# Optimization experiments

Hardware: AMD Instinct MI355X
Metric: run time of the kernel (lower is better)

Reference implementation:

```python
import jax, jax.numpy as jnp
import numpy as np

B, N, M, NS = 4, 32768, 1024, 32
RADIUS = 0.1
EPS = 1e-5
CHANS = [16, 32, 32, 64]


def setup_inputs() -> dict:
    key = jax.random.key(0)
    ks = jax.random.split(key, 8)
    d = {
        'theta': jax.random.uniform(ks[0], (B, N), jnp.float32, 0.0, float(np.pi)),
        'phi': jax.random.uniform(ks[1], (B, N), jnp.float32, 0.0, 2.0 * float(np.pi)),
        'features': jax.random.normal(ks[2], (B, CHANS[0], N), jnp.float32),
    }
    for i, (ci, co) in enumerate(zip(CHANS[:-1], CHANS[1:])):
        d[f'w{i}'] = jax.random.normal(jax.random.fold_in(ks[3], i), (co, ci), jnp.float32) * 0.1
        d[f'b{i}'] = jnp.zeros((co,), jnp.float32)
        d[f'g{i}'] = jnp.ones((co,), jnp.float32)
        d[f'be{i}'] = jnp.zeros((co,), jnp.float32)
    return d


def _group(theta, phi, features):
    # angular ball query + random neighbor sampling (deterministic key),
    # duplicates padded with the first valid neighbor (max-pool invariant,
    # matching the torch code's sampling-with-replacement semantics).
    k1, k2 = jax.random.split(jax.random.key(42))
    n = theta.shape[1]
    cent_idx = jax.random.permutation(k1, n)[:M]                 # shared across batch, like torch code
    ct = theta[:, cent_idx]                                      # (B, M)
    cp = phi[:, cent_idx]
    th_s, ph_s = jax.lax.stop_gradient(theta), jax.lax.stop_gradient(phi)
    ct_s, cp_s = jax.lax.stop_gradient(ct), jax.lax.stop_gradient(cp)
    dist = jnp.sqrt((th_s[:, None, :] - ct_s[:, :, None]) ** 2 +
                    (ph_s[:, None, :] - cp_s[:, :, None]) ** 2)  # (B, M, N)
    mask = dist <= RADIUS
    scores = jnp.where(mask, jax.random.uniform(k2, dist.shape, jnp.float32), jnp.inf)
    _, idx = jax.lax.top_k(-scores, NS)                          # NS random in-ball indices, (B, M, NS)
    valid = jnp.take_along_axis(mask, idx, axis=-1)
    idx = jnp.where(valid, idx, idx[..., :1])                    # centroid itself is always valid at slot 0
    gathered = jax.vmap(lambda f, i: f[:, i])(features, idx)     # (B, C, M, NS)
    grouped = jnp.transpose(gathered, (0, 1, 3, 2))              # (B, C, NS, M)
    return ct, cp, grouped


def _mlp_max(x, params):
    # 1x1 conv + BatchNorm (batch stats, training mode) + ReLU stack, then max over nsample
    for w, b, g, be in params:
        x = jnp.einsum('oc,bcsm->bosm', w, x) + b[None, :, None, None]
        mu = x.mean(axis=(0, 2, 3), keepdims=True)
        var = x.var(axis=(0, 2, 3), keepdims=True)
        x = (x - mu) * jax.lax.rsqrt(var + EPS) * g[None, :, None, None] + be[None, :, None, None]
        x = jax.nn.relu(x)
    return x.max(axis=2)                                         # (B, C_out, M)


def reference(theta, phi, features, w0, b0, g0, be0, w1, b1, g1, be1, w2, b2, g2, be2):
    params = [(w0, b0, g0, be0), (w1, b1, g1, be1), (w2, b2, g2, be2)]
    ct, cp, grouped = _group(theta, phi, features)
    new_feats = _mlp_max(grouped, params)
    return ct, cp, new_feats
```

## Files before the change

kernel.cpp:

```cpp
#include <hip/hip_runtime.h>
#include <stdint.h>

#define N_PTS 32768
#define M_CENT 1024
#define B_SZ 4
#define NS 32
#define NR 64
#define P_TOT (B_SZ * NS * M_CENT)

#define GT 29
#define GP 58
#define NCELL (GT * GP)
#define INVF (1.0f / 0.11f)
#define CAPW 320

__device__ __forceinline__ int cell_t(float t) {
  return min(GT - 1, (int)(t * INVF));
}
__device__ __forceinline__ int cell_p(float p) {
  return min(GP - 1, (int)(p * INVF));
}

struct Key2 { uint32_t a, b; };

__device__ __forceinline__ uint32_t rotl32(uint32_t v, uint32_t r) {
  return (v << r) | (v >> (32u - r));
}

__device__ __forceinline__ void tf2x32(uint32_t k0, uint32_t k1,
                                       uint32_t& x0, uint32_t& x1) {
  uint32_t ks0 = k0, ks1 = k1, ks2 = k0 ^ k1 ^ 0x1BD11BDAu;
  x0 += ks0; x1 += ks1;
#define TF_ROUND(r) { x0 += x1; x1 = rotl32(x1, r); x1 ^= x0; }
  TF_ROUND(13u) TF_ROUND(15u) TF_ROUND(26u) TF_ROUND(6u)
  x0 += ks1; x1 += ks2 + 1u;
  TF_ROUND(17u) TF_ROUND(29u) TF_ROUND(16u) TF_ROUND(24u)
  x0 += ks2; x1 += ks0 + 2u;
  TF_ROUND(13u) TF_ROUND(15u) TF_ROUND(26u) TF_ROUND(6u)
  x0 += ks0; x1 += ks1 + 3u;
  TF_ROUND(17u) TF_ROUND(29u) TF_ROUND(16u) TF_ROUND(24u)
  x0 += ks1; x1 += ks2 + 4u;
  TF_ROUND(13u) TF_ROUND(15u) TF_ROUND(26u) TF_ROUND(6u)
  x0 += ks2; x1 += ks0 + 5u;
#undef TF_ROUND
}

__device__ __forceinline__ Key2 tf_block(Key2 k, uint32_t hi, uint32_t lo) {
  uint32_t x0 = hi, x1 = lo;
  tf2x32(k.a, k.b, x0, x1);
  Key2 r; r.a = x0; r.b = x1; return r;
}

__global__ __launch_bounds__(256) void prep_kernel(const float* __restrict__ theta,
                                                   const float* __restrict__ phi,
                                                   uint32_t* __restrict__ bits1,
                                                   uint32_t* __restrict__ bits2,
                                                   int* __restrict__ hist1,
                                                   int* __restrict__ hist2,
                                                   int* __restrict__ cellcnt) {
  int j = blockIdx.x * 256 + threadIdx.x;
  int b = j >> 15;
  float t = theta[j], p = phi[j];
  atomicAdd(&cellcnt[b * NCELL + cell_t(t) * GP + cell_p(p)], 1);
  if (j < N_PTS) {
    Key2 root; root.a = 0u; root.b = 42u;
    Key2 k1   = tf_block(root, 0u, 0u);
    Key2 keyA = tf_block(k1, 0u, 0u);
    Key2 sub1 = tf_block(k1, 0u, 1u);
    Key2 sub2 = tf_block(keyA, 0u, 1u);
    Key2 r1 = tf_block(sub1, 0u, (uint32_t)j);
    Key2 r2 = tf_block(sub2, 0u, (uint32_t)j);
    uint32_t v1 = r1.a ^ r1.b, v2 = r2.a ^ r2.b;
    bits1[j] = v1; bits2[j] = v2;
    atomicAdd(&hist1[v1 >> 16], 1);
    atomicAdd(&hist2[v2 >> 16], 1);
  }
}

__global__ __launch_bounds__(256) void transpose_kernel(const float* __restrict__ feat,
                                                        float* __restrict__ featT) {
  __shared__ float lds[16][65];
  int b = blockIdx.y;
  int n0 = blockIdx.x * 64;
  int tid = threadIdx.x;
#pragma unroll
  for (int k = 0; k < 4; ++k) {
    int v = tid + k * 256;
    int c = v >> 6, no = v & 63;
    lds[c][no] = feat[((size_t)(b * 16 + c) << 15) + n0 + no];
  }
  __syncthreads();
#pragma unroll
  for (int k = 0; k < 4; ++k) {
    int v = tid + k * 256;
    int no = v >> 4, c = v & 15;
    featT[((size_t)(b << 15) + n0 + no) * 16 + c] = lds[c][no];
  }
}

__global__ __launch_bounds__(256) void scans_kernel(const int* __restrict__ hist1,
                                                    const int* __restrict__ hist2,
                                                    int* __restrict__ gbase1,
                                                    int* __restrict__ gbase2,
                                                    const int* __restrict__ cellcnt,
                                                    int* __restrict__ cellpre,
                                                    int* __restrict__ cellcur) {
  __shared__ int s[256];
  int t = threadIdx.x;
  if (blockIdx.x < 2) {
    const int* hist = blockIdx.x == 0 ? hist1 : hist2;
    int* gbase = blockIdx.x == 0 ? gbase1 : gbase2;
    int sum = 0;
    for (int i = 0; i < 256; ++i) sum += hist[t * 256 + i];
    s[t] = sum;
    __syncthreads();
    if (t == 0) {
      int run = 0;
      for (int i = 0; i < 256; ++i) { int v = s[i]; s[i] = run; run += v; }
    }
    __syncthreads();
    gbase[t] = s[t];
  } else {
    int b = blockIdx.x - 2;
    const int* cnt = cellcnt + b * NCELL;
    int i0 = t * 7, i1 = min(i0 + 7, NCELL);
    int sum = 0;
    for (int i = i0; i < i1; ++i) sum += cnt[i];
    s[t] = sum;
    __syncthreads();
    for (int off = 1; off < 256; off <<= 1) {
      int v = (t >= off) ? s[t - off] : 0;
      __syncthreads();
      s[t] += v;
      __syncthreads();
    }
    int run = (t == 0) ? 0 : s[t - 1];
    for (int i = i0; i < i1; ++i) {
      cellpre[b * NCELL + i] = run;
      cellcur[b * NCELL + i] = run;
      run += cnt[i];
    }
  }
}

__global__ __launch_bounds__(256) void bucket_scan_kernel(const int* __restrict__ hist1,
                                                          const int* __restrict__ hist2,
                                                          const int* __restrict__ gbase1,
                                                          const int* __restrict__ gbase2,
                                                          int* __restrict__ prefix1,
                                                          int* __restrict__ prefix2,
                                                          int* __restrict__ cursor1,
                                                          int* __restrict__ cursor2) {
  __shared__ int s[256];
  const int* hist = blockIdx.y == 0 ? hist1 : hist2;
  const int* gbase = blockIdx.y == 0 ? gbase1 : gbase2;
  int* prefix = blockIdx.y == 0 ? prefix1 : prefix2;
  int* cursor = blockIdx.y == 0 ? cursor1 : cursor2;
  int g = blockIdx.x, t = threadIdx.x;
  int idx = g * 256 + t;
  int orig = hist[idx];
  s[t] = orig;
  __syncthreads();
  for (int off = 1; off < 256; off <<= 1) {
    int v = (t >= off) ? s[t - off] : 0;
    __syncthreads();
    s[t] += v;
    __syncthreads();
  }
  int pref = gbase[g] + s[t] - orig;
  prefix[idx] = pref;
  cursor[idx] = pref;
}

__global__ __launch_bounds__(256) void scatter_kernel(const float* __restrict__ theta,
                                                      const float* __restrict__ phi,
                                                      int* __restrict__ cellcur,
                                                      float4* __restrict__ pts4,
                                                      const uint32_t* __restrict__ bits1,
                                                      const uint32_t* __restrict__ bits2,
                                                      int* __restrict__ cursor1,
                                                      int* __restrict__ cursor2,
                                                      int* __restrict__ sorted1,
                                                      int* __restrict__ sorted2) {
  int j = blockIdx.x * 256 + threadIdx.x;
  int b = j >> 15, n = j & (N_PTS - 1);
  float t = theta[j], p = phi[j];
  int cell = b * NCELL + cell_t(t) * GP + cell_p(p);
  int pos = atomicAdd(&cellcur[cell], 1);
  pts4[(b << 15) + pos] = make_float4(t, p, __int_as_float(n), 0.0f);
  if (j < N_PTS) {
    int p1 = atomicAdd(&cursor1[bits1[j] >> 16], 1);
    sorted1[p1] = j;
    int p2 = atomicAdd(&cursor2[bits2[j] >> 16], 1);
    sorted2[p2] = j;
  }
}

__device__ __forceinline__ int exact_rank(const uint32_t* __restrict__ bits,
                                          const int* __restrict__ prefix,
                                          const int* __restrict__ hist,
                                          const int* __restrict__ sorted, int j) {
  uint32_t my = bits[j];
  int b = (int)(my >> 16);
  int start = prefix[b];
  int cnt = hist[b];
  int r = start;
  for (int i = 0; i < cnt; ++i) {
    int m = sorted[start + i];
    uint32_t vb = bits[m];
    if (vb < my || (vb == my && m < j)) ++r;
  }
  return r;
}

__global__ __launch_bounds__(256) void rank_scatter1_kernel(
    const uint32_t* __restrict__ bits1, const uint32_t* __restrict__ bits2,
    const int* __restrict__ prefix1, const int* __restrict__ prefix2,
    const int* __restrict__ hist1, const int* __restrict__ hist2,
    const int* __restrict__ sorted1, const int* __restrict__ sorted2,
    int* __restrict__ xmid, int* __restrict__ rank2) {
  int j = blockIdx.x * 256 + threadIdx.x;
  int r1 = exact_rank(bits1, prefix1, hist1, sorted1, j);
  xmid[r1] = j;
  rank2[j] = exact_rank(bits2, prefix2, hist2, sorted2, j);
}

__global__ __launch_bounds__(256) void scatter2_kernel(const int* __restrict__ rank2,
                                                       const int* __restrict__ xmid,
                                                       int* __restrict__ xfin) {
  int p = blockIdx.x * 256 + threadIdx.x;
  xfin[rank2[p]] = xmid[p];
}

__global__ __launch_bounds__(256) void select_kernel(
    const float* __restrict__ theta, const float* __restrict__ phi,
    const int* __restrict__ cent,
    const int* __restrict__ cellpre, const int* __restrict__ cellcnt,
    const float4* __restrict__ pts4,
    int* __restrict__ idx_buf, float* __restrict__ out_ct, float* __restrict__ out_cp) {
  __shared__ float wsc[4][CAPW];
  __shared__ int wsn[4][CAPW];
  int tid = threadIdx.x;
  int w = tid >> 6, lane = tid & 63;
  int bm = blockIdx.x * 4 + w;
  int b = bm >> 10, m = bm & 1023;
  int ci = cent[m];
  float ctv = theta[(b << 15) + ci];
  float cpv = phi[(b << 15) + ci];
  if (lane == 0) { out_ct[bm] = ctv; out_cp[bm] = cpv; }

  Key2 root; root.a = 0u; root.b = 42u;
  Key2 k2 = tf_block(root, 0u, 1u);
  uint32_t flat_base = (uint32_t)bm << 15;

  int tc = cell_t(ctv), pc = cell_p(cpv);
  int t0 = max(0, tc - 1), t1 = min(GT - 1, tc + 1);
  int p0 = max(0, pc - 1), p1 = min(GP - 1, pc + 1);
  int nct = t1 - t0 + 1, ncp = p1 - p0 + 1, ncells = nct * ncp;

  int cst = 0, ccn = 0;
  if (lane < ncells) {
    int cell = b * NCELL + (t0 + lane / ncp) * GP + (p0 + lane % ncp);
    cst = cellpre[cell];
    ccn = cellcnt[cell];
  }
  int sc9[9], cc9[9];
#pragma unroll
  for (int k = 0; k < 9; ++k) {
    sc9[k] = __shfl(cst, k);
    cc9[k] = __shfl(ccn, k);
  }
  int T = 0;
#pragma unroll
  for (int k = 0; k < 9; ++k) T += cc9[k];

  const float4* bpts = pts4 + ((size_t)b << 15);
  int wcnt = 0;
  for (int base = 0; base < T; base += 64) {
    int i = base + lane;
    bool hit = false; float sc = 0.0f; int n = 0;
    if (i < T) {
      int gidx = 0, acc = 0;
#pragma unroll
      for (int k = 0; k < 9; ++k) {
        int lo = acc; acc += cc9[k];
        if (i >= lo && i < acc) gidx = sc9[k] + (i - lo);
      }
      float4 pt = bpts[gidx];
      float dx = __fsub_rn(pt.x, ctv);
      float dy = __fsub_rn(pt.y, cpv);
      float d = __fsqrt_rn(__fadd_rn(__fmul_rn(dx, dx), __fmul_rn(dy, dy)));
      if (d <= 0.1f) {
        hit = true; n = __float_as_int(pt.z);
        Key2 r = tf_block(k2, 0u, flat_base + (uint32_t)n);
        uint32_t bits = r.a ^ r.b;
        sc = __uint_as_float(0x3f800000u | (bits >> 9)) - 1.0f;
      }
    }
    unsigned long long mask = __ballot(hit);
    int pos = wcnt + __popcll(mask & ((1ull << lane) - 1ull));
    if (hit && pos < CAPW) { wsc[w][pos] = sc; wsn[w][pos] = n; }
    wcnt = min(wcnt + (int)__popcll(mask), CAPW);
  }

  int mysel;
  if (wcnt <= 64) {
    float s = (lane < wcnt) ? wsc[w][lane] : 3.0e38f;
    int n = (lane < wcnt) ? wsn[w][lane] : 0x7fffffff;
#pragma unroll
    for (int k = 2; k <= 64; k <<= 1) {
#pragma unroll
      for (int jj = k >> 1; jj > 0; jj >>= 1) {
        float os = __shfl_xor(s, jj);
        int on = __shfl_xor(n, jj);
        bool lower = (lane & jj) == 0;
        bool dir = (lane & k) == 0;
        bool mineFirst = (s < os) || (s == os && n < on);
        bool takeMine = ((lower == mineFirst) == dir);
        s = takeMine ? s : os;
        n = takeMine ? n : on;
      }
    }
    int n0 = __shfl(n, 0);
    mysel = (lane < wcnt) ? n : n0;
  } else {
    float ls = -1.0f; int ln = -1;
    int sel0 = -1; mysel = -1;
    for (int r = 0; r < NS; ++r) {
      float best = 3.0e38f; int bn = 0x7fffffff;
      for (int i = lane; i < wcnt; i += 64) {
        float s = wsc[w][i]; int n = wsn[w][i];
        bool after = (s > ls) || (s == ls && n > ln);
        bool better = (s < best) || (s == best && n < bn);
        if (after && better) { best = s; bn = n; }
      }
      for (int off = 32; off; off >>= 1) {
        float os = __shfl_xor(best, off);
        int on = __shfl_xor(bn, off);
        if (os < best || (os == best && on < bn)) { best = os; bn = on; }
      }
      int chosen;
      if (best < 3.0e38f) { ls = best; ln = bn; chosen = bn; }
      else chosen = sel0;
      if (r == 0) sel0 = chosen;
      if (lane == r) mysel = chosen;
    }
  }
  if (lane < NS) idx_buf[bm * NS + lane] = mysel;
}

__device__ __forceinline__ float bn_relu(float y, float mu, float r, float g, float be) {
  float t = __fsub_rn(y, mu);
  t = __fmul_rn(t, r);
  t = __fmul_rn(t, g);
  t = __fadd_rn(t, be);
  return fmaxf(t, 0.0f);
}

__global__ __launch_bounds__(256) void l1_kernel(
    const float* __restrict__ feat, const float* __restrict__ featT,
    const int* __restrict__ idx_buf,
    const float* __restrict__ w0, const float* __restrict__ b0,
    float* __restrict__ Y1g, double* __restrict__ stats, int useT) {
  int j = blockIdx.x * 256 + threadIdx.x;
  int bm = j >> 5, s = j & 31, b = bm >> 10;
  int lane = threadIdx.x & 63;
  int idx = idx_buf[j];
  float x[16];
  if (useT) {
    const float4* src = reinterpret_cast<const float4*>(
        featT + (((size_t)b << 15) + (size_t)idx) * 16);
#pragma unroll
    for (int q = 0; q < 4; ++q) {
      float4 f = src[q];
      x[q * 4 + 0] = f.x; x[q * 4 + 1] = f.y;
      x[q * 4 + 2] = f.z; x[q * 4 + 3] = f.w;
    }
  } else {
#pragma unroll
    for (int c = 0; c < 16; ++c)
      x[c] = feat[((size_t)(b * 16 + c) << 15) + idx];
  }
  float y[32];
#pragma unroll
  for (int o = 0; o < 32; ++o) {
    float acc = b0[o];
#pragma unroll
    for (int c = 0; c < 16; ++c) acc = fmaf(w0[o * 16 + c], x[c], acc);
    y[o] = acc;
    Y1g[(size_t)bm * 1024 + o * 32 + s] = acc;
  }
  int rep = (j >> 6) & (NR - 1);
  double* base = stats + (size_t)rep * 64;
#pragma unroll
  for (int o = 0; o < 32; ++o) {
    float s1 = y[o], s2 = y[o] * y[o];
#pragma unroll
    for (int off = 32; off; off >>= 1) {
      s1 += __shfl_xor(s1, off);
      s2 += __shfl_xor(s2, off);
    }
    if (lane == 0) {
      atomicAdd(base + o, (double)s1);
      atomicAdd(base + 32 + o, (double)s2);
    }
  }
}

__global__ __launch_bounds__(256) void l2_kernel(
    const float* __restrict__ Y1g,
    const float* __restrict__ mur1, const float* __restrict__ g0, const float* __restrict__ be0,
    const float* __restrict__ w1, const float* __restrict__ b1,
    double* __restrict__ stats) {
  int j = blockIdx.x * 256 + threadIdx.x;
  int bm = j >> 5, s = j & 31;
  int lane = threadIdx.x & 63;
  float x2[32];
#pragma unroll
  for (int c = 0; c < 32; ++c)
    x2[c] = bn_relu(Y1g[(size_t)bm * 1024 + c * 32 + s],
                    mur1[c], mur1[32 + c], g0[c], be0[c]);
  int rep = (j >> 6) & (NR - 1);
  double* base = stats + (size_t)rep * 64;
#pragma unroll
  for (int o = 0; o < 32; ++o) {
    float acc = b1[o];
#pragma unroll
    for (int c = 0; c < 32; ++c) acc = fmaf(w1[o * 32 + c], x2[c], acc);
    float s1 = acc, s2 = acc * acc;
#pragma unroll
    for (int off = 32; off; off >>= 1) {
      s1 += __shfl_xor(s1, off);
      s2 += __shfl_xor(s2, off);
    }
    if (lane == 0) {
      atomicAdd(base + o, (double)s1);
      atomicAdd(base + 32 + o, (double)s2);
    }
  }
}

__global__ __launch_bounds__(256) void l3_kernel(
    const float* __restrict__ Y1g,
    const float* __restrict__ mur1, const float* __restrict__ g0, const float* __restrict__ be0,
    const float* __restrict__ w1, const float* __restrict__ b1,
    const float* __restrict__ mur2, const float* __restrict__ g1, const float* __restrict__ be1,
    const float* __restrict__ w2, const float* __restrict__ b2,
    float* __restrict__ mm3, double* __restrict__ stats) {
  int j = blockIdx.x * 256 + threadIdx.x;
  int bm = j >> 5, s = j & 31;
  int lane = threadIdx.x & 63;
  float x2[32];
#pragma unroll
  for (int c = 0; c < 32; ++c)
    x2[c] = bn_relu(Y1g[(size_t)bm * 1024 + c * 32 + s],
                    mur1[c], mur1[32 + c], g0[c], be0[c]);
  float x3[32];
#pragma unroll
  for (int o = 0; o < 32; ++o) {
    float acc = b1[o];
#pragma unroll
    for (int c = 0; c < 32; ++c) acc = fmaf(w1[o * 32 + c], x2[c], acc);
    x3[o] = bn_relu(acc, mur2[o], mur2[32 + o], g1[o], be1[o]);
  }
  int rep = (j >> 6) & (NR - 1);
  double* base = stats + (size_t)rep * 128;
#pragma unroll
  for (int o = 0; o < 64; ++o) {
    float acc = b2[o];
#pragma unroll
    for (int c = 0; c < 32; ++c) acc = fmaf(w2[o * 32 + c], x3[c], acc);
    float s1 = acc, s2 = acc * acc;
#pragma unroll
    for (int off = 32; off; off >>= 1) {
      s1 += __shfl_xor(s1, off);
      s2 += __shfl_xor(s2, off);
    }
    if (lane == 0) {
      atomicAdd(base + o, (double)s1);
      atomicAdd(base + 64 + o, (double)s2);
    }
    float mx = acc, mn = acc;
#pragma unroll
    for (int off = 16; off; off >>= 1) {
      mx = fmaxf(mx, __shfl_xor(mx, off));
      mn = fminf(mn, __shfl_xor(mn, off));
    }
    if (s == 0) {
      mm3[bm * 128 + o * 2] = mx;
      mm3[bm * 128 + o * 2 + 1] = mn;
    }
  }
}

__global__ __launch_bounds__(256) void final_small_kernel(
    const float* __restrict__ mm3,
    const float* __restrict__ mur3, const float* __restrict__ g2, const float* __restrict__ be2,
    float* __restrict__ out_ft) {
  int j = blockIdx.x * 256 + threadIdx.x;
  int b = j >> 16, o = (j >> 10) & 63, m = j & 1023;
  int bm = b * 1024 + m;
  float g = g2[o];
  float y = (g >= 0.0f) ? mm3[bm * 128 + o * 2] : mm3[bm * 128 + o * 2 + 1];
  out_ft[j] = bn_relu(y, mur3[o], mur3[64 + o], g, be2[o]);
}

template <int CO>
__global__ void fixup_mur_kernel(const double* __restrict__ S, float* __restrict__ mur) {
  int o = threadIdx.x;
  if (o >= CO) return;
  double s1 = 0.0, s2 = 0.0;
  for (int r = 0; r < NR; ++r) {
    s1 += S[r * 2 * CO + o];
    s2 += S[r * 2 * CO + CO + o];
  }
  const double P = (double)P_TOT;
  double mu = s1 / P;
  double var = s2 / P - mu * mu;
  mur[o] = (float)mu;
  mur[CO + o] = (float)(1.0 / sqrt(var + 1e-5));
}

extern "C" void kernel_launch(void* const* d_in, const int* in_sizes, int n_in,
                              void* d_out, int out_size, void* d_ws, size_t ws_size,
                              hipStream_t stream) {
  (void)in_sizes; (void)n_in; (void)out_size;
  const float* theta = (const float*)d_in[0];
  const float* phi   = (const float*)d_in[1];
  const float* feat  = (const float*)d_in[2];
  const float* w0 = (const float*)d_in[3];
  const float* b0 = (const float*)d_in[4];
  const float* g0 = (const float*)d_in[5];
  const float* be0 = (const float*)d_in[6];
  const float* w1 = (const float*)d_in[7];
  const float* b1 = (const float*)d_in[8];
  const float* g1 = (const float*)d_in[9];
  const float* be1 = (const float*)d_in[10];
  const float* w2 = (const float*)d_in[11];
  const float* b2 = (const float*)d_in[12];
  const float* g2 = (const float*)d_in[13];
  const float* be2 = (const float*)d_in[14];

  float* out = (float*)d_out;
  float* out_ct = out;
  float* out_cp = out + B_SZ * M_CENT;
  float* out_ft = out + 2 * B_SZ * M_CENT;

  char* ws = (char*)d_ws;
  uint32_t* bits1 = (uint32_t*)(ws + 0);
  uint32_t* bits2 = (uint32_t*)(ws + 131072);
  int* rank2 = (int*)(ws + 262144);
  int* xmid  = (int*)(ws + 393216);
  int* xfin  = (int*)(ws + 524288);
  int* idx_buf = (int*)(ws + 655360);
  int* hist1   = (int*)(ws + 1179648);
  int* hist2   = (int*)(ws + 1441792);
  int* cellcnt = (int*)(ws + 1703936);
  double* stats1 = (double*)(ws + 1736704);
  double* stats2 = (double*)(ws + 1769472);
  double* stats3 = (double*)(ws + 1802240);
  int* prefix1 = (int*)(ws + 1867776);
  int* prefix2 = (int*)(ws + 2129920);
  int* cursor1 = (int*)(ws + 2392064);
  int* cursor2 = (int*)(ws + 2654208);
  int* sorted1 = (int*)(ws + 2916352);
  int* sorted2 = (int*)(ws + 3047424);
  int* gbase1  = (int*)(ws + 3178496);
  int* gbase2  = (int*)(ws + 3179520);
  int* cellpre = (int*)(ws + 3180544);
  int* cellcur = (int*)(ws + 3213312);
  float4* pts4 = (float4*)(ws + 3246080);
  float* mur1 = (float*)(ws + 5343232);
  float* mur2 = (float*)(ws + 5343488);
  float* mur3 = (float*)(ws + 5343744);
  float* mm3  = (float*)(ws + 5344768);
  float* Y1g  = (float*)(ws + 7441920);
  float* featT = (float*)(ws + 7441920 + 16777216);
  size_t NEED_T = (size_t)7441920 + 16777216 + 8388608;
  int useT = (ws_size >= NEED_T) ? 1 : 0;

  hipMemsetAsync(ws + 1179648, 0, 688128, stream);

  prep_kernel<<<512, 256, 0, stream>>>(theta, phi, bits1, bits2, hist1, hist2, cellcnt);
  if (useT)
    transpose_kernel<<<dim3(512, 4), 256, 0, stream>>>(feat, featT);
  scans_kernel<<<6, 256, 0, stream>>>(hist1, hist2, gbase1, gbase2,
                                      cellcnt, cellpre, cellcur);
  bucket_scan_kernel<<<dim3(256, 2), 256, 0, stream>>>(hist1, hist2, gbase1, gbase2,
                                                       prefix1, prefix2, cursor1, cursor2);
  scatter_kernel<<<512, 256, 0, stream>>>(theta, phi, cellcur, pts4,
                                          bits1, bits2, cursor1, cursor2,
                                          sorted1, sorted2);
  rank_scatter1_kernel<<<128, 256, 0, stream>>>(bits1, bits2, prefix1, prefix2,
                                                hist1, hist2, sorted1, sorted2,
                                                xmid, rank2);
  scatter2_kernel<<<128, 256, 0, stream>>>(rank2, xmid, xfin);

  select_kernel<<<1024, 256, 0, stream>>>(theta, phi, xfin, cellpre, cellcnt,
                                          pts4, idx_buf, out_ct, out_cp);

  l1_kernel<<<512, 256, 0, stream>>>(feat, featT, idx_buf, w0, b0, Y1g, stats1, useT);
  fixup_mur_kernel<32><<<1, 64, 0, stream>>>(stats1, mur1);
  l2_kernel<<<512, 256, 0, stream>>>(Y1g, mur1, g0, be0, w1, b1, stats2);
  fixup_mur_kernel<32><<<1, 64, 0, stream>>>(stats2, mur2);
  l3_kernel<<<512, 256, 0, stream>>>(Y1g, mur1, g0, be0, w1, b1,
                                     mur2, g1, be1, w2, b2, mm3, stats3);
  fixup_mur_kernel<64><<<1, 64, 0, stream>>>(stats3, mur3);
  final_small_kernel<<<1024, 256, 0, stream>>>(mm3, mur3, g2, be2, out_ft);
}
```

Before: 288.4 us.

## Split MLP output channels across thread halves and reduce BN stats via shared memory

Each of the three MLP kernels now gives every point to two threads, each computing half of the output channels, and doubles the grid size. Per-channel sum, sum-of-squares and max/min reductions move from wave-wide shuffle loops with per-wave double atomics to a shared-memory transpose, where each thread reduces one channel over a segment of points and issues far fewer atomics. This is meant to cut shuffle and atomic overhead and raise parallelism. In exchange it adds shared-memory traffic, block barriers, and in l2/l3 each thread of the pair recomputes the full input activation vector.

```diff
diff --git a/kernel.cpp b/kernel.cpp
--- a/kernel.cpp
+++ b/kernel.cpp
@@ -362,10 +362,12 @@
     const int* __restrict__ idx_buf,
     const float* __restrict__ w0, const float* __restrict__ b0,
     float* __restrict__ Y1g, double* __restrict__ stats, int useT) {
-  int j = blockIdx.x * 256 + threadIdx.x;
-  int bm = j >> 5, s = j & 31, b = bm >> 10;
-  int lane = threadIdx.x & 63;
-  int idx = idx_buf[j];
+  __shared__ float y1s[128 * 34];
+  int tid = threadIdx.x;
+  int pl = tid & 127, h = tid >> 7;
+  int pg = blockIdx.x * 128 + pl;
+  int bm = pg >> 5, s = pg & 31, b = bm >> 10;
+  int idx = idx_buf[pg];
   float x[16];
   if (useT) {
     const float4* src = reinterpret_cast<const float4*>(
@@ -381,30 +383,26 @@
     for (int c = 0; c < 16; ++c)
       x[c] = feat[((size_t)(b * 16 + c) << 15) + idx];
   }
-  float y[32];
-#pragma unroll
-  for (int o = 0; o < 32; ++o) {
+#pragma unroll
+  for (int oo = 0; oo < 16; ++oo) {
+    int o = h * 16 + oo;
     float acc = b0[o];
 #pragma unroll
     for (int c = 0; c < 16; ++c) acc = fmaf(w0[o * 16 + c], x[c], acc);
-    y[o] = acc;
     Y1g[(size_t)bm * 1024 + o * 32 + s] = acc;
-  }
-  int rep = (j >> 6) & (NR - 1);
-  double* base = stats + (size_t)rep * 64;
-#pragma unroll
-  for (int o = 0; o < 32; ++o) {
-    float s1 = y[o], s2 = y[o] * y[o];
-#pragma unroll
-    for (int off = 32; off; off >>= 1) {
-      s1 += __shfl_xor(s1, off);
-      s2 += __shfl_xor(s2, off);
-    }
-    if (lane == 0) {
-      atomicAdd(base + o, (double)s1);
-      atomicAdd(base + 32 + o, (double)s2);
-    }
-  }
+    y1s[pl * 34 + o] = acc;
+  }
+  __syncthreads();
+  int ch = tid & 31, seg = tid >> 5;
+  float s1 = 0.0f, s2 = 0.0f;
+#pragma unroll
+  for (int i = 0; i < 16; ++i) {
+    float v = y1s[(seg * 16 + i) * 34 + ch];
+    s1 += v; s2 += v * v;
+  }
+  double* base = stats + (size_t)(blockIdx.x & (NR - 1)) * 64;
+  atomicAdd(base + ch, (double)s1);
+  atomicAdd(base + 32 + ch, (double)s2);
 }
 
 __global__ __launch_bounds__(256) void l2_kernel(
@@ -412,32 +410,35 @@
     const float* __restrict__ mur1, const float* __restrict__ g0, const float* __restrict__ be0,
     const float* __restrict__ w1, const float* __restrict__ b1,
     double* __restrict__ stats) {
-  int j = blockIdx.x * 256 + threadIdx.x;
-  int bm = j >> 5, s = j & 31;
-  int lane = threadIdx.x & 63;
+  __shared__ float y2s[128 * 34];
+  int tid = threadIdx.x;
+  int pl = tid & 127, h = tid >> 7;
+  int pg = blockIdx.x * 128 + pl;
+  int bm = pg >> 5, s = pg & 31;
   float x2[32];
 #pragma unroll
   for (int c = 0; c < 32; ++c)
     x2[c] = bn_relu(Y1g[(size_t)bm * 1024 + c * 32 + s],
                     mur1[c], mur1[32 + c], g0[c], be0[c]);
-  int rep = (j >> 6) & (NR - 1);
-  double* base = stats + (size_t)rep * 64;
-#pragma unroll
-  for (int o = 0; o < 32; ++o) {
+#pragma unroll
+  for (int oo = 0; oo < 16; ++oo) {
+    int o = h * 16 + oo;
     float acc = b1[o];
 #pragma unroll
     for (int c = 0; c < 32; ++c) acc = fmaf(w1[o * 32 + c], x2[c], acc);
-    float s1 = acc, s2 = acc * acc;
-#pragma unroll
-    for (int off = 32; off; off >>= 1) {
-      s1 += __shfl_xor(s1, off);
-      s2 += __shfl_xor(s2, off);
-    }
-    if (lane == 0) {
-      atomicAdd(base + o, (double)s1);
-      atomicAdd(base + 32 + o, (double)s2);
-    }
-  }
+    y2s[pl * 34 + o] = acc;
+  }
+  __syncthreads();
+  int ch = tid & 31, seg = tid >> 5;
+  float s1 = 0.0f, s2 = 0.0f;
+#pragma unroll
+  for (int i = 0; i < 16; ++i) {
+    float v = y2s[(seg * 16 + i) * 34 + ch];
+    s1 += v; s2 += v * v;
+  }
+  double* base = stats + (size_t)(blockIdx.x & (NR - 1)) * 64;
+  atomicAdd(base + ch, (double)s1);
+  atomicAdd(base + 32 + ch, (double)s2);
 }
 
 __global__ __launch_bounds__(256) void l3_kernel(
@@ -447,50 +448,52 @@
     const float* __restrict__ mur2, const float* __restrict__ g1, const float* __restrict__ be1,
     const float* __restrict__ w2, const float* __restrict__ b2,
     float* __restrict__ mm3, double* __restrict__ stats) {
-  int j = blockIdx.x * 256 + threadIdx.x;
-  int bm = j >> 5, s = j & 31;
-  int lane = threadIdx.x & 63;
+  __shared__ float smem[128 * 66];
+  int tid = threadIdx.x;
+  int pl = tid & 127, h = tid >> 7;
+  int pg = blockIdx.x * 128 + pl;
+  int bm = pg >> 5, s = pg & 31;
   float x2[32];
 #pragma unroll
   for (int c = 0; c < 32; ++c)
     x2[c] = bn_relu(Y1g[(size_t)bm * 1024 + c * 32 + s],
                     mur1[c], mur1[32 + c], g0[c], be0[c]);
+#pragma unroll
+  for (int cc = 0; cc < 16; ++cc) {
+    int c = h * 16 + cc;
+    float acc = b1[c];
+#pragma unroll
+    for (int k = 0; k < 32; ++k) acc = fmaf(w1[c * 32 + k], x2[k], acc);
+    smem[pl * 34 + c] = bn_relu(acc, mur2[c], mur2[32 + c], g1[c], be1[c]);
+  }
+  __syncthreads();
   float x3[32];
 #pragma unroll
-  for (int o = 0; o < 32; ++o) {
-    float acc = b1[o];
-#pragma unroll
-    for (int c = 0; c < 32; ++c) acc = fmaf(w1[o * 32 + c], x2[c], acc);
-    x3[o] = bn_relu(acc, mur2[o], mur2[32 + o], g1[o], be1[o]);
-  }
-  int rep = (j >> 6) & (NR - 1);
-  double* base = stats + (size_t)rep * 128;
-#pragma unroll
-  for (int o = 0; o < 64; ++o) {
+  for (int c = 0; c < 32; ++c) x3[c] = smem[pl * 34 + c];
+  __syncthreads();
+#pragma unroll
+  for (int oo = 0; oo < 32; ++oo) {
+    int o = h * 32 + oo;
     float acc = b2[o];
 #pragma unroll
     for (int c = 0; c < 32; ++c) acc = fmaf(w2[o * 32 + c], x3[c], acc);
-    float s1 = acc, s2 = acc * acc;
-#pragma unroll
-    for (int off = 32; off; off >>= 1) {
-      s1 += __shfl_xor(s1, off);
-      s2 += __shfl_xor(s2, off);
-    }
-    if (lane == 0) {
-      atomicAdd(base + o, (double)s1);
-      atomicAdd(base + 64 + o, (double)s2);
-    }
-    float mx = acc, mn = acc;
-#pragma unroll
-    for (int off = 16; off; off >>= 1) {
-      mx = fmaxf(mx, __shfl_xor(mx, off));
-      mn = fminf(mn, __shfl_xor(mn, off));
-    }
-    if (s == 0) {
-      mm3[bm * 128 + o * 2] = mx;
-      mm3[bm * 128 + o * 2 + 1] = mn;
-    }
-  }
+    smem[pl * 66 + o] = acc;
+  }
+  __syncthreads();
+  int ch = tid & 63, bmq = tid >> 6;
+  float s1 = 0.0f, s2 = 0.0f, mx = -3.0e38f, mn = 3.0e38f;
+#pragma unroll
+  for (int i = 0; i < 32; ++i) {
+    float v = smem[(bmq * 32 + i) * 66 + ch];
+    s1 += v; s2 += v * v;
+    mx = fmaxf(mx, v); mn = fminf(mn, v);
+  }
+  double* base = stats + (size_t)(blockIdx.x & (NR - 1)) * 128;
+  atomicAdd(base + ch, (double)s1);
+  atomicAdd(base + 64 + ch, (double)s2);
+  int bmg = blockIdx.x * 4 + bmq;
+  mm3[bmg * 128 + ch * 2] = mx;
+  mm3[bmg * 128 + ch * 2 + 1] = mn;
 }
 
 __global__ __launch_bounds__(256) void final_small_kernel(
@@ -599,12 +602,12 @@
   select_kernel<<<1024, 256, 0, stream>>>(theta, phi, xfin, cellpre, cellcnt,
                                           pts4, idx_buf, out_ct, out_cp);
 
-  l1_kernel<<<512, 256, 0, stream>>>(feat, featT, idx_buf, w0, b0, Y1g, stats1, useT);
+  l1_kernel<<<1024, 256, 0, stream>>>(feat, featT, idx_buf, w0, b0, Y1g, stats1, useT);
   fixup_mur_kernel<32><<<1, 64, 0, stream>>>(stats1, mur1);
-  l2_kernel<<<512, 256, 0, stream>>>(Y1g, mur1, g0, be0, w1, b1, stats2);
+  l2_kernel<<<1024, 256, 0, stream>>>(Y1g, mur1, g0, be0, w1, b1, stats2);
   fixup_mur_kernel<32><<<1, 64, 0, stream>>>(stats2, mur2);
-  l3_kernel<<<512, 256, 0, stream>>>(Y1g, mur1, g0, be0, w1, b1,
-                                     mur2, g1, be1, w2, b2, mm3, stats3);
+  l3_kernel<<<1024, 256, 0, stream>>>(Y1g, mur1, g0, be0, w1, b1,
+                                      mur2, g1, be1, w2, b2, mm3, stats3);
   fixup_mur_kernel<64><<<1, 64, 0, stream>>>(stats3, mur3);
   final_small_kernel<<<1024, 256, 0, stream>>>(mm3, mur3, g2, be2, out_ft);
 }
```

Result: faster. 276.9 us (-4.0%).
